# Optimization experiments

Measured on AMD Instinct MI355X. Metric: run time of the kernel, lower is better.

The kernel has to match this reference:

```python
import jax, jax.numpy as jnp
import numpy as np

NEG_SLOPE = 0.2  # PyG GATv2Conv default negative_slope
N_NODES = 50000
N_EDGES = 600000
N_GRAPHS = 512


def gatv2_layer(x, src, dst, Wl, bl, Wr, br, att, bias, n_nodes, heads, out_ch):
    """PyG GATv2Conv (concat=False -> mean over heads). src/dst include self-loops."""
    xl = (x @ Wl + bl).reshape(n_nodes, heads, out_ch)  # source transform
    xr = (x @ Wr + br).reshape(n_nodes, heads, out_ch)  # target transform
    e = jax.nn.leaky_relu(xl[src] + xr[dst], NEG_SLOPE)          # [E, H, C]
    logits = jnp.einsum('ehc,hc->eh', e, att)                     # [E, H]
    # segment softmax over destination node
    amax = jax.ops.segment_max(logits, dst, num_segments=n_nodes)  # [N, H]
    amax = jnp.where(jnp.isfinite(amax), amax, 0.0)
    ex = jnp.exp(logits - amax[dst])
    denom = jax.ops.segment_sum(ex, dst, num_segments=n_nodes)
    alpha = ex / jnp.clip(denom[dst], 1e-16)                      # [E, H]
    msg = xl[src] * alpha[:, :, None]                             # [E, H, C]
    out = jax.ops.segment_sum(msg, dst, num_segments=n_nodes)     # [N, H, C]
    return out.mean(axis=1) + bias                                # [N, C]


def setup_inputs() -> dict:
    key = jax.random.key(0)
    ks = jax.random.split(key, 20)
    s = 0.1
    x = jax.random.normal(ks[0], (N_NODES, 7), dtype=jnp.float32)
    edge_index = jax.random.randint(ks[1], (2, N_EDGES), 0, N_NODES, dtype=jnp.int64)
    batch = jnp.sort(jax.random.randint(ks[2], (N_NODES,), 0, N_GRAPHS, dtype=jnp.int64))
    H1, C1 = 2, 64   # conv1: 7 -> 64, heads=2
    H2, C2 = 2, 64   # conv2: 64 -> 64, heads=2
    H3, C3 = 1, 128  # conv3: 64 -> 128, heads=1
    p = {
        'W1l': jax.random.normal(ks[3], (7, H1 * C1)) * s,
        'b1l': jnp.zeros((H1 * C1,), jnp.float32),
        'W1r': jax.random.normal(ks[4], (7, H1 * C1)) * s,
        'b1r': jnp.zeros((H1 * C1,), jnp.float32),
        'att1': jax.random.normal(ks[5], (H1, C1)) * s,
        'bias1': jnp.zeros((C1,), jnp.float32),
        'W2l': jax.random.normal(ks[6], (C1, H2 * C2)) * s,
        'b2l': jnp.zeros((H2 * C2,), jnp.float32),
        'W2r': jax.random.normal(ks[7], (C1, H2 * C2)) * s,
        'b2r': jnp.zeros((H2 * C2,), jnp.float32),
        'att2': jax.random.normal(ks[8], (H2, C2)) * s,
        'bias2': jnp.zeros((C2,), jnp.float32),
        'W3l': jax.random.normal(ks[9], (C2, H3 * C3)) * s,
        'b3l': jnp.zeros((H3 * C3,), jnp.float32),
        'W3r': jax.random.normal(ks[10], (C2, H3 * C3)) * s,
        'b3r': jnp.zeros((H3 * C3,), jnp.float32),
        'att3': jax.random.normal(ks[11], (H3, C3)) * s,
        'bias3': jnp.zeros((C3,), jnp.float32),
        'Wc': jax.random.normal(ks[12], (C3, 11)) * s,
        'bc': jnp.zeros((11,), jnp.float32),
    }
    return {'x': x, 'edge_index': edge_index, 'batch': batch, **p}


def reference(x, edge_index, batch,
              W1l, b1l, W1r, b1r, att1, bias1,
              W2l, b2l, W2r, b2r, att2, bias2,
              W3l, b3l, W3r, b3r, att3, bias3,
              Wc, bc):
    n = x.shape[0]
    # GATv2Conv default add_self_loops=True (same augmented edge set each layer)
    loop = jnp.arange(n, dtype=edge_index.dtype)
    src = jnp.concatenate([edge_index[0], loop])
    dst = jnp.concatenate([edge_index[1], loop])

    h = jax.nn.elu(gatv2_layer(x, src, dst, W1l, b1l, W1r, b1r, att1, bias1, n, 2, 64))
    h = jax.nn.elu(gatv2_layer(h, src, dst, W2l, b2l, W2r, b2r, att2, bias2, n, 2, 64))
    h = gatv2_layer(h, src, dst, W3l, b3l, W3r, b3r, att3, bias3, n, 1, 128)

    # global mean pool over graphs
    sums = jax.ops.segment_sum(h, batch, num_segments=N_GRAPHS)          # [G, 128]
    cnt = jax.ops.segment_sum(jnp.ones((n,), h.dtype), batch, num_segments=N_GRAPHS)
    graph_embed = sums / jnp.clip(cnt, 1.0)[:, None]
    return graph_embed @ Wc + bc                                         # [G, 11]
```

## Files before the change

### kernel.cpp

```cpp
#include <hip/hip_runtime.h>
#include <hip/hip_bf16.h>
#include <math.h>


#define PAD_SHIFT 6


__global__ void build_csr(const int* __restrict__ edge_src, const int* __restrict__ edge_dst,
                          int* __restrict__ cnt, int* __restrict__ csr, int NE, int E) {
    int e = blockIdx.x * blockDim.x + threadIdx.x;
    if (e >= E) return;
    int s, d;
    if (e < NE) { s = edge_src[e]; d = edge_dst[e]; }
    else        { s = d = e - NE; }
    int pos = atomicAdd(&cnt[d], 1) & 63;
    csr[(d << PAD_SHIFT) + pos] = s;
}


template<int IN_CH, int NPW>
__global__ __launch_bounds__(256) void transform_tile(
        const float* __restrict__ in,
        const float* __restrict__ Wl, const float* __restrict__ bl,
        const float* __restrict__ Wr, const float* __restrict__ br,
        ushort* __restrict__ xlh, float* __restrict__ xr, int n) {
    constexpr int NPB = 4 * NPW;
    __shared__ alignas(16) float rows[NPB][IN_CH];
    int tid = threadIdx.x;
    int t = tid & 63, w = tid >> 6;
    int n0 = blockIdx.x * NPB;

    if constexpr (IN_CH % 4 == 0) {
        constexpr int K4 = IN_CH / 4;
        for (int idx = tid; idx < NPB * K4; idx += 256) {
            int nn = idx / K4, k4 = idx - nn * K4;
            int node = n0 + nn; if (node > n - 1) node = n - 1;
            ((float4*)rows[nn])[k4] = ((const float4*)(in + (size_t)node * IN_CH))[k4];
        }
    } else {
        for (int idx = tid; idx < NPB * IN_CH; idx += 256) {
            int nn = idx / IN_CH, k = idx - nn * IN_CH;
            int node = n0 + nn; if (node > n - 1) node = n - 1;
            rows[nn][k] = in[(size_t)node * IN_CH + k];
        }
    }
    __syncthreads();

    int nb = w * NPW;
    float accl0[NPW], accl1[NPW], accr0[NPW], accr1[NPW];
    float bl0 = bl[t], bl1 = bl[t + 64], br0 = br[t], br1 = br[t + 64];
#pragma unroll
    for (int nn = 0; nn < NPW; ++nn) {
        accl0[nn] = bl0; accl1[nn] = bl1; accr0[nn] = br0; accr1[nn] = br1;
    }

    if constexpr (IN_CH % 4 == 0) {
        constexpr int K4 = IN_CH / 4;
        for (int k4 = 0; k4 < K4; ++k4) {
            float wl0[4], wl1[4], wr0[4], wr1[4];
#pragma unroll
            for (int j = 0; j < 4; ++j) {
                wl0[j] = Wl[(k4 * 4 + j) * 128 + t];
                wl1[j] = Wl[(k4 * 4 + j) * 128 + t + 64];
                wr0[j] = Wr[(k4 * 4 + j) * 128 + t];
                wr1[j] = Wr[(k4 * 4 + j) * 128 + t + 64];
            }
#pragma unroll
            for (int nn = 0; nn < NPW; ++nn) {
                float4 r = ((const float4*)rows[nb + nn])[k4];
                accl0[nn] = fmaf(r.x, wl0[0], accl0[nn]);
                accl1[nn] = fmaf(r.x, wl1[0], accl1[nn]);
                accr0[nn] = fmaf(r.x, wr0[0], accr0[nn]);
                accr1[nn] = fmaf(r.x, wr1[0], accr1[nn]);
                accl0[nn] = fmaf(r.y, wl0[1], accl0[nn]);
                accl1[nn] = fmaf(r.y, wl1[1], accl1[nn]);
                accr0[nn] = fmaf(r.y, wr0[1], accr0[nn]);
                accr1[nn] = fmaf(r.y, wr1[1], accr1[nn]);
                accl0[nn] = fmaf(r.z, wl0[2], accl0[nn]);
                accl1[nn] = fmaf(r.z, wl1[2], accl1[nn]);
                accr0[nn] = fmaf(r.z, wr0[2], accr0[nn]);
                accr1[nn] = fmaf(r.z, wr1[2], accr1[nn]);
                accl0[nn] = fmaf(r.w, wl0[3], accl0[nn]);
                accl1[nn] = fmaf(r.w, wl1[3], accl1[nn]);
                accr0[nn] = fmaf(r.w, wr0[3], accr0[nn]);
                accr1[nn] = fmaf(r.w, wr1[3], accr1[nn]);
            }
        }
    } else {
#pragma unroll
        for (int k = 0; k < IN_CH; ++k) {
            float wl0 = Wl[k * 128 + t], wl1 = Wl[k * 128 + t + 64];
            float wr0 = Wr[k * 128 + t], wr1 = Wr[k * 128 + t + 64];
#pragma unroll
            for (int nn = 0; nn < NPW; ++nn) {
                float xv = rows[nb + nn][k];
                accl0[nn] = fmaf(xv, wl0, accl0[nn]);
                accl1[nn] = fmaf(xv, wl1, accl1[nn]);
                accr0[nn] = fmaf(xv, wr0, accr0[nn]);
                accr1[nn] = fmaf(xv, wr1, accr1[nn]);
            }
        }
    }

#pragma unroll
    for (int nn = 0; nn < NPW; ++nn) {
        int node = n0 + nb + nn;
        if (node < n) {
            __hip_bfloat16* hl = (__hip_bfloat16*)(xlh + ((size_t)node << 7));
            float* orr = xr + ((size_t)node << 7);
            hl[t]      = __float2bfloat16(accl0[nn]);
            hl[t + 64] = __float2bfloat16(accl1[nn]);
            orr[t] = accr0[nn]; orr[t + 64] = accr1[nn];
        }
    }
}


template<int CTRL>
__device__ __forceinline__ float dpp_add(float v) {
    int x = __builtin_amdgcn_update_dpp(0, __float_as_int(v), CTRL, 0xF, 0xF, true);
    return v + __int_as_float(x);
}
__device__ __forceinline__ float reduce16(float v) {
    v = dpp_add<0xB1>(v);
    v = dpp_add<0x4E>(v);
    v = dpp_add<0x141>(v);
    v = dpp_add<0x140>(v);
    return v;
}


__device__ __forceinline__ void unpack4(const uint2& u, float c[4]) {
    c[0] = __int_as_float((int)(u.x << 16));
    c[1] = __int_as_float((int)(u.x & 0xffff0000u));
    c[2] = __int_as_float((int)(u.y << 16));
    c[3] = __int_as_float((int)(u.y & 0xffff0000u));
}


__device__ __forceinline__ float chan4v(float p, const float c[4], const float xv[4],
                                        const float a[4], const float a2[4]) {
#pragma unroll
    for (int k = 0; k < 4; ++k) {
        float t = c[k] + xv[k];
        p = fmaf(t > 0.f ? a[k] : a2[k], t, p);
    }
    return p;
}
__device__ __forceinline__ void acc4v(float acc[4], float w, const float c[4]) {
#pragma unroll
    for (int k = 0; k < 4; ++k) acc[k] = fmaf(w, c[k], acc[k]);
}


#define AGG_PH(CUR0, CUR1, FRE0, FRE1)                                         \
    {                                                                          \
        int tf0 = srcof(it + 2 * EPI + eg);                                    \
        int tf1 = srcof(it + 2 * EPI + STEP + eg);                             \
        FRE0[0] = *(const uint2*)(xlh + ((size_t)tf0 << 7) + rowo);            \
        FRE0[1] = *(const uint2*)(xlh + ((size_t)tf1 << 7) + rowo);            \
        if constexpr (!TWOHEAD) {                                              \
            FRE1[0] = *(const uint2*)(xlh + ((size_t)tf0 << 7) + rowo + 64);   \
            FRE1[1] = *(const uint2*)(xlh + ((size_t)tf1 << 7) + rowo + 64);   \
        }                                                                      \
        bool v0 = (it + eg) < deg, v1 = (it + STEP + eg) < deg;                \
        float ca[4], cb[4], da[4], db[4];                                      \
        unpack4(CUR0[0], ca); unpack4(CUR0[1], cb);                            \
        float pa = chan4v(0.f, ca, xrv0, atv0, atw0);                          \
        float pb = chan4v(0.f, cb, xrv0, atv0, atw0);                          \
        if constexpr (!TWOHEAD) {                                              \
            unpack4(CUR1[0], da); unpack4(CUR1[1], db);                        \
            pa = chan4v(pa, da, xrv1, atv1, atw1);                             \
            pb = chan4v(pb, db, xrv1, atv1, atw1);                             \
        }                                                                      \
        pa = reduce16(pa); pb = reduce16(pb);                                  \
        float w0 = v0 ? exp2f(pa) : 0.f;                                       \
        float w1 = v1 ? exp2f(pb) : 0.f;                                       \
        ssum += w0 + w1;                                                       \
        acc4v(acc0, w0, ca); acc4v(acc0, w1, cb);                              \
        if constexpr (!TWOHEAD) { acc4v(acc1, w0, da); acc4v(acc1, w1, db); }  \
        it += EPI;                                                             \
    }

template<bool TWOHEAD>
__global__ void gat_agg_fused(const ushort* __restrict__ xlh, const float* __restrict__ xr,
                              const float* __restrict__ att, const float* __restrict__ bias,
                              const int* __restrict__ cnt, const int* __restrict__ csr,
                              float* __restrict__ outbuf, int n) {
    constexpr int STEP = TWOHEAD ? 2 : 4;
    constexpr int EPI  = 2 * STEP;
    constexpr float L2E = 1.4426950408889634f;
    int wid = (blockIdx.x * blockDim.x + threadIdx.x) >> 6;
    if (wid >= n) return;
    int node = wid;
    int lane = threadIdx.x & 63;
    int g = lane >> 4, q = lane & 15;
    int eg   = TWOHEAD ? (g >> 1) : g;
    int head = TWOHEAD ? (g & 1)  : 0;
    int rowo = TWOHEAD ? (head * 64 + q * 4) : (q * 4);

    float xrv0[4], atv0[4], atw0[4], acc0[4];
    float xrv1[4], atv1[4], atw1[4], acc1[4];
    {
        float4 x0 = *(const float4*)(xr + ((size_t)node << 7) + rowo);
        float4 a0 = *(const float4*)(att + rowo);
        xrv0[0]=x0.x; xrv0[1]=x0.y; xrv0[2]=x0.z; xrv0[3]=x0.w;
        atv0[0]=a0.x*L2E; atv0[1]=a0.y*L2E; atv0[2]=a0.z*L2E; atv0[3]=a0.w*L2E;
#pragma unroll
        for (int k = 0; k < 4; ++k) { atw0[k] = 0.2f * atv0[k]; acc0[k] = 0.f; }
        if constexpr (!TWOHEAD) {
            float4 x1 = *(const float4*)(xr + ((size_t)node << 7) + rowo + 64);
            float4 a1 = *(const float4*)(att + rowo + 64);
            xrv1[0]=x1.x; xrv1[1]=x1.y; xrv1[2]=x1.z; xrv1[3]=x1.w;
            atv1[0]=a1.x*L2E; atv1[1]=a1.y*L2E; atv1[2]=a1.z*L2E; atv1[3]=a1.w*L2E;
#pragma unroll
            for (int k = 0; k < 4; ++k) { atw1[k] = 0.2f * atv1[k]; acc1[k] = 0.f; }
        }
    }

    int deg = cnt[node]; if (deg > 64) deg = 64;
    int idxvec = csr[((size_t)node << PAD_SHIFT) + lane];
    auto srcof = [&](int p) { return __shfl(idxvec, p < deg ? p : 0, 64); };

    uint2 X0[2], X1[2], Y0[2], Y1[2], Z0[2], Z1[2];
    {
        int s00 = srcof(eg), s01 = srcof(STEP + eg);
        int s10 = srcof(EPI + eg), s11 = srcof(EPI + STEP + eg);
        X0[0] = *(const uint2*)(xlh + ((size_t)s00 << 7) + rowo);
        X0[1] = *(const uint2*)(xlh + ((size_t)s01 << 7) + rowo);
        Y0[0] = *(const uint2*)(xlh + ((size_t)s10 << 7) + rowo);
        Y0[1] = *(const uint2*)(xlh + ((size_t)s11 << 7) + rowo);
        if constexpr (!TWOHEAD) {
            X1[0] = *(const uint2*)(xlh + ((size_t)s00 << 7) + rowo + 64);
            X1[1] = *(const uint2*)(xlh + ((size_t)s01 << 7) + rowo + 64);
            Y1[0] = *(const uint2*)(xlh + ((size_t)s10 << 7) + rowo + 64);
            Y1[1] = *(const uint2*)(xlh + ((size_t)s11 << 7) + rowo + 64);
        }
    }

    float ssum = 0.f;
    int it = 0;
    while (true) {
        AGG_PH(X0, X1, Z0, Z1)
        if (it >= deg) break;
        AGG_PH(Y0, Y1, X0, X1)
        if (it >= deg) break;
        AGG_PH(Z0, Z1, Y0, Y1)
        if (it >= deg) break;
    }

    ssum += __shfl_xor(ssum, 32, 64);
#pragma unroll
    for (int k = 0; k < 4; ++k) acc0[k] += __shfl_xor(acc0[k], 32, 64);
    if constexpr (!TWOHEAD) {
        ssum += __shfl_xor(ssum, 16, 64);
#pragma unroll
        for (int k = 0; k < 4; ++k) {
            acc1[k] += __shfl_xor(acc1[k], 32, 64);
            acc0[k] += __shfl_xor(acc0[k], 16, 64);
            acc1[k] += __shfl_xor(acc1[k], 16, 64);
        }
    }

    float inv = 1.f / ssum;
    if constexpr (TWOHEAD) {
        float o[4];
#pragma unroll
        for (int k = 0; k < 4; ++k) {
            float r = acc0[k] * inv;
            float ro = __shfl_xor(r, 16, 64);
            float v = 0.5f * (r + ro) + bias[q * 4 + k];
            o[k] = (v > 0.f) ? v : expm1f(v);
        }
        if (lane < 16)
            ((float4*)(outbuf + (size_t)node * 64))[q] = make_float4(o[0], o[1], o[2], o[3]);
    } else {
        float o0[4], o1[4];
#pragma unroll
        for (int k = 0; k < 4; ++k) {
            o0[k] = acc0[k] * inv + bias[q * 4 + k];
            o1[k] = acc1[k] * inv + bias[q * 4 + 64 + k];
        }
        if (lane < 16) {
            float4* op = (float4*)(outbuf + ((size_t)node << 7));
            op[q]      = make_float4(o0[0], o0[1], o0[2], o0[3]);
            op[q + 16] = make_float4(o1[0], o1[1], o1[2], o1[3]);
        }
    }
}


__device__ __forceinline__ int lower_bound(const int* __restrict__ a, int n, int key) {
    int lo = 0, hi = n;
    while (lo < hi) {
        int mid = (lo + hi) >> 1;
        if (a[mid] < key) lo = mid + 1; else hi = mid;
    }
    return lo;
}

__global__ void pool_kernel(const float* __restrict__ h3, const int* __restrict__ batch,
                            const float* __restrict__ Wc, const float* __restrict__ bc,
                            float* __restrict__ out, int n, int G) {
    int g = blockIdx.x;
    int tid = threadIdx.x;
    __shared__ float mean[128];
    int start = lower_bound(batch, n, g);
    int end   = lower_bound(batch, n, g + 1);
    float s0 = 0.f, s1 = 0.f, s2 = 0.f, s3 = 0.f;
    int node = start;
    for (; node + 3 < end; node += 4) {
        s0 += h3[(size_t)node * 128 + tid];
        s1 += h3[(size_t)(node + 1) * 128 + tid];
        s2 += h3[(size_t)(node + 2) * 128 + tid];
        s3 += h3[(size_t)(node + 3) * 128 + tid];
    }
    for (; node < end; ++node) s0 += h3[(size_t)node * 128 + tid];
    float s = (s0 + s1) + (s2 + s3);
    int cnt = end - start;
    float mv = s / (float)(cnt > 0 ? cnt : 1);
    mean[tid] = mv;
    __syncthreads();
    if (tid < 11) {
        float o = bc[tid];
        for (int c = 0; c < 128; ++c) o += mean[c] * Wc[c * 11 + tid];
        out[g * 11 + tid] = o;
    }
}


extern "C" void kernel_launch(void* const* d_in, const int* in_sizes, int n_in,
                              void* d_out, int out_size, void* d_ws, size_t ws_size,
                              hipStream_t stream) {
    const float* x     = (const float*)d_in[0];
    const int*   ei    = (const int*)d_in[1];
    const int*   batch = (const int*)d_in[2];
    const float* W1l = (const float*)d_in[3],  *b1l = (const float*)d_in[4];
    const float* W1r = (const float*)d_in[5],  *b1r = (const float*)d_in[6];
    const float* att1 = (const float*)d_in[7], *bias1 = (const float*)d_in[8];
    const float* W2l = (const float*)d_in[9],  *b2l = (const float*)d_in[10];
    const float* W2r = (const float*)d_in[11], *b2r = (const float*)d_in[12];
    const float* att2 = (const float*)d_in[13], *bias2 = (const float*)d_in[14];
    const float* W3l = (const float*)d_in[15], *b3l = (const float*)d_in[16];
    const float* W3r = (const float*)d_in[17], *b3r = (const float*)d_in[18];
    const float* att3 = (const float*)d_in[19], *bias3 = (const float*)d_in[20];
    const float* Wc  = (const float*)d_in[21], *bc  = (const float*)d_in[22];
    float* out = (float*)d_out;

    const int N  = in_sizes[0] / 7;
    const int NE = in_sizes[1] / 2;
    const int E  = NE + N;
    const int G  = out_size / 11;

    const int* edge_src = ei;
    const int* edge_dst = ei + NE;

    char* p = (char*)d_ws;
    auto alloc = [&](size_t bytes) { void* r = (void*)p; p += (bytes + 255) & ~(size_t)255; return r; };
    int*    cnt  = (int*)alloc((size_t)N * sizeof(int));
    int*    csr  = (int*)alloc((size_t)N * 64 * sizeof(int));
    ushort* xlh  = (ushort*)alloc((size_t)N * 128 * sizeof(ushort));
    float*  xr   = (float*)alloc((size_t)N * 128 * sizeof(float));
    float*  hbuf = (float*)alloc((size_t)N * 128 * sizeof(float));

    (void)hipMemsetAsync(cnt, 0, (size_t)N * sizeof(int), stream);
    build_csr<<<(E + 255) / 256, 256, 0, stream>>>(edge_src, edge_dst, cnt, csr, NE, E);

    const int NPB = 32;
    int tgrid = (N + NPB - 1) / NPB;
    int agrid = (N + 3) / 4;

    transform_tile<7, 8><<<tgrid, 256, 0, stream>>>(x, W1l, b1l, W1r, b1r, xlh, xr, N);
    gat_agg_fused<true><<<agrid, 256, 0, stream>>>(xlh, xr, att1, bias1, cnt, csr, hbuf, N);

    transform_tile<64, 8><<<tgrid, 256, 0, stream>>>(hbuf, W2l, b2l, W2r, b2r, xlh, xr, N);
    gat_agg_fused<true><<<agrid, 256, 0, stream>>>(xlh, xr, att2, bias2, cnt, csr, hbuf, N);

    transform_tile<64, 8><<<tgrid, 256, 0, stream>>>(hbuf, W3l, b3l, W3r, b3r, xlh, xr, N);
    gat_agg_fused<false><<<agrid, 256, 0, stream>>>(xlh, xr, att3, bias3, cnt, csr, hbuf, N);

    pool_kernel<<<G, 128, 0, stream>>>(hbuf, batch, Wc, bc, out, N, G);
}
```

Before: 248.4 us.

## Use abs-based leaky-relu logits, skip masked loads, split pooling across two halves

The per-channel leaky-relu select becomes a branch-free form, 0.6*a*t + 0.4*a*|t|, with constants prefolded. The aggregation loop now skips prefetch loads and validity masks on full iterations and only masks the tail. The pool kernel uses 256 threads, so two halves sum node ranges in parallel and combine through shared memory. These changes aim to cut per-edge ALU work and redundant tail loads, and to shorten the serial reduction per graph, at the cost of more branching in the loop.

```diff
diff --git a/kernel.cpp b/kernel.cpp
--- a/kernel.cpp
+++ b/kernel.cpp
@@ -138,14 +138,16 @@
 }
 
 
-__device__ __forceinline__ float chan4v(float p, const float c[4], const float xv[4],
-                                        const float a[4], const float a2[4]) {
+__device__ __forceinline__ float chanA(const float c[4], const float xv[4],
+                                       const float aA[4], const float aB[4]) {
+    float p1 = 0.f, p2 = 0.f;
 #pragma unroll
     for (int k = 0; k < 4; ++k) {
         float t = c[k] + xv[k];
-        p = fmaf(t > 0.f ? a[k] : a2[k], t, p);
-    }
-    return p;
+        p1 = fmaf(aA[k], t, p1);
+        p2 = fmaf(aB[k], fabsf(t), p2);
+    }
+    return p1 + p2;
 }
 __device__ __forceinline__ void acc4v(float acc[4], float w, const float c[4]) {
 #pragma unroll
@@ -153,8 +155,7 @@
 }
 
 
-#define AGG_PH(CUR0, CUR1, FRE0, FRE1)                                         \
-    {                                                                          \
+#define AGG_LOADF(FRE0, FRE1)                                                  \
         int tf0 = srcof(it + 2 * EPI + eg);                                    \
         int tf1 = srcof(it + 2 * EPI + STEP + eg);                             \
         FRE0[0] = *(const uint2*)(xlh + ((size_t)tf0 << 7) + rowo);            \
@@ -162,24 +163,37 @@
         if constexpr (!TWOHEAD) {                                              \
             FRE1[0] = *(const uint2*)(xlh + ((size_t)tf0 << 7) + rowo + 64);   \
             FRE1[1] = *(const uint2*)(xlh + ((size_t)tf1 << 7) + rowo + 64);   \
-        }                                                                      \
-        bool v0 = (it + eg) < deg, v1 = (it + STEP + eg) < deg;                \
+        }
+
+#define AGG_COMPUTE(CUR0, CUR1, MASKED)                                        \
         float ca[4], cb[4], da[4], db[4];                                      \
         unpack4(CUR0[0], ca); unpack4(CUR0[1], cb);                            \
-        float pa = chan4v(0.f, ca, xrv0, atv0, atw0);                          \
-        float pb = chan4v(0.f, cb, xrv0, atv0, atw0);                          \
+        float pa = chanA(ca, xrv0, atA0, atB0);                                \
+        float pb = chanA(cb, xrv0, atA0, atB0);                                \
         if constexpr (!TWOHEAD) {                                              \
             unpack4(CUR1[0], da); unpack4(CUR1[1], db);                        \
-            pa = chan4v(pa, da, xrv1, atv1, atw1);                             \
-            pb = chan4v(pb, db, xrv1, atv1, atw1);                             \
+            pa += chanA(da, xrv1, atA1, atB1);                                 \
+            pb += chanA(db, xrv1, atA1, atB1);                                 \
         }                                                                      \
         pa = reduce16(pa); pb = reduce16(pb);                                  \
-        float w0 = v0 ? exp2f(pa) : 0.f;                                       \
-        float w1 = v1 ? exp2f(pb) : 0.f;                                       \
+        float w0, w1;                                                          \
+        if (MASKED) {                                                          \
+            w0 = (it + eg) < deg ? exp2f(pa) : 0.f;                            \
+            w1 = (it + STEP + eg) < deg ? exp2f(pb) : 0.f;                     \
+        } else { w0 = exp2f(pa); w1 = exp2f(pb); }                             \
         ssum += w0 + w1;                                                       \
         acc4v(acc0, w0, ca); acc4v(acc0, w1, cb);                              \
         if constexpr (!TWOHEAD) { acc4v(acc1, w0, da); acc4v(acc1, w1, db); }  \
-        it += EPI;                                                             \
+        it += EPI;
+
+#define AGG_STEP(CUR0, CUR1, FRE0, FRE1)                                       \
+    {                                                                          \
+        if (it + EPI <= deg) {                                                 \
+            AGG_LOADF(FRE0, FRE1)                                              \
+            AGG_COMPUTE(CUR0, CUR1, false)                                     \
+        } else if (it < deg) {                                                 \
+            AGG_COMPUTE(CUR0, CUR1, true)                                      \
+        } else break;                                                          \
     }
 
 template<bool TWOHEAD>
@@ -199,22 +213,30 @@
     int head = TWOHEAD ? (g & 1)  : 0;
     int rowo = TWOHEAD ? (head * 64 + q * 4) : (q * 4);
 
-    float xrv0[4], atv0[4], atw0[4], acc0[4];
-    float xrv1[4], atv1[4], atw1[4], acc1[4];
+    float xrv0[4], atA0[4], atB0[4], acc0[4];
+    float xrv1[4], atA1[4], atB1[4], acc1[4];
     {
         float4 x0 = *(const float4*)(xr + ((size_t)node << 7) + rowo);
         float4 a0 = *(const float4*)(att + rowo);
+        float av0[4] = { a0.x, a0.y, a0.z, a0.w };
         xrv0[0]=x0.x; xrv0[1]=x0.y; xrv0[2]=x0.z; xrv0[3]=x0.w;
-        atv0[0]=a0.x*L2E; atv0[1]=a0.y*L2E; atv0[2]=a0.z*L2E; atv0[3]=a0.w*L2E;
-#pragma unroll
-        for (int k = 0; k < 4; ++k) { atw0[k] = 0.2f * atv0[k]; acc0[k] = 0.f; }
+#pragma unroll
+        for (int k = 0; k < 4; ++k) {
+            atA0[k] = 0.6f * L2E * av0[k];
+            atB0[k] = 0.4f * L2E * av0[k];
+            acc0[k] = 0.f;
+        }
         if constexpr (!TWOHEAD) {
             float4 x1 = *(const float4*)(xr + ((size_t)node << 7) + rowo + 64);
             float4 a1 = *(const float4*)(att + rowo + 64);
+            float av1[4] = { a1.x, a1.y, a1.z, a1.w };
             xrv1[0]=x1.x; xrv1[1]=x1.y; xrv1[2]=x1.z; xrv1[3]=x1.w;
-            atv1[0]=a1.x*L2E; atv1[1]=a1.y*L2E; atv1[2]=a1.z*L2E; atv1[3]=a1.w*L2E;
-#pragma unroll
-            for (int k = 0; k < 4; ++k) { atw1[k] = 0.2f * atv1[k]; acc1[k] = 0.f; }
+#pragma unroll
+            for (int k = 0; k < 4; ++k) {
+                atA1[k] = 0.6f * L2E * av1[k];
+                atB1[k] = 0.4f * L2E * av1[k];
+                acc1[k] = 0.f;
+            }
         }
     }
 
@@ -241,12 +263,9 @@
     float ssum = 0.f;
     int it = 0;
     while (true) {
-        AGG_PH(X0, X1, Z0, Z1)
-        if (it >= deg) break;
-        AGG_PH(Y0, Y1, X0, X1)
-        if (it >= deg) break;
-        AGG_PH(Z0, Z1, Y0, Y1)
-        if (it >= deg) break;
+        AGG_STEP(X0, X1, Z0, Z1)
+        AGG_STEP(Y0, Y1, X0, X1)
+        AGG_STEP(Z0, Z1, Y0, Y1)
     }
 
     ssum += __shfl_xor(ssum, 32, 64);
@@ -299,31 +318,35 @@
     return lo;
 }
 
-__global__ void pool_kernel(const float* __restrict__ h3, const int* __restrict__ batch,
-                            const float* __restrict__ Wc, const float* __restrict__ bc,
-                            float* __restrict__ out, int n, int G) {
+__global__ __launch_bounds__(256) void pool_kernel(
+        const float* __restrict__ h3, const int* __restrict__ batch,
+        const float* __restrict__ Wc, const float* __restrict__ bc,
+        float* __restrict__ out, int n, int G) {
     int g = blockIdx.x;
     int tid = threadIdx.x;
+    int c = tid & 127, half = tid >> 7;
+    __shared__ float partial[2][128];
     __shared__ float mean[128];
     int start = lower_bound(batch, n, g);
     int end   = lower_bound(batch, n, g + 1);
-    float s0 = 0.f, s1 = 0.f, s2 = 0.f, s3 = 0.f;
-    int node = start;
-    for (; node + 3 < end; node += 4) {
-        s0 += h3[(size_t)node * 128 + tid];
-        s1 += h3[(size_t)(node + 1) * 128 + tid];
-        s2 += h3[(size_t)(node + 2) * 128 + tid];
-        s3 += h3[(size_t)(node + 3) * 128 + tid];
-    }
-    for (; node < end; ++node) s0 += h3[(size_t)node * 128 + tid];
-    float s = (s0 + s1) + (s2 + s3);
-    int cnt = end - start;
-    float mv = s / (float)(cnt > 0 ? cnt : 1);
-    mean[tid] = mv;
+    int cnt   = end - start;
+    int mid   = start + (cnt >> 1);
+    int lo = half ? mid : start;
+    int hi = half ? end : mid;
+    float s0 = 0.f, s1 = 0.f;
+    int node = lo;
+    for (; node + 1 < hi; node += 2) {
+        s0 += h3[(size_t)node * 128 + c];
+        s1 += h3[(size_t)(node + 1) * 128 + c];
+    }
+    if (node < hi) s0 += h3[(size_t)node * 128 + c];
+    partial[half][c] = s0 + s1;
+    __syncthreads();
+    if (tid < 128) mean[tid] = (partial[0][tid] + partial[1][tid]) / (float)(cnt > 0 ? cnt : 1);
     __syncthreads();
     if (tid < 11) {
         float o = bc[tid];
-        for (int c = 0; c < 128; ++c) o += mean[c] * Wc[c * 11 + tid];
+        for (int cc = 0; cc < 128; ++cc) o += mean[cc] * Wc[cc * 11 + tid];
         out[g * 11 + tid] = o;
     }
 }
@@ -379,5 +402,5 @@
     transform_tile<64, 8><<<tgrid, 256, 0, stream>>>(hbuf, W3l, b3l, W3r, b3r, xlh, xr, N);
     gat_agg_fused<false><<<agrid, 256, 0, stream>>>(xlh, xr, att3, bias3, cnt, csr, hbuf, N);
 
-    pool_kernel<<<G, 128, 0, stream>>>(hbuf, batch, Wc, bc, out, N, G);
-}
+    pool_kernel<<<G, 256, 0, stream>>>(hbuf, batch, Wc, bc, out, N, G);
+}
```

After: 255.7 us. 3.0% more time.
